# Kernel optimization log

Hardware: AMD Instinct MI355X
Metric: run time of the kernel (lower is better)

The kernel has to match this reference:

```python
import jax, jax.numpy as jnp
import numpy as np

ALPHA = 0.99
EPS = 1e-12
INIT_HI = -60.0
INIT_LO = -90.0
VAR0 = 40.0 ** 2


def setup_inputs() -> dict:
    key = jax.random.key(0)
    x = jax.random.normal(key, (256, 4000, 64), dtype=jnp.float32)
    return {"x": x}


def reference(x) -> jnp.ndarray:
    B, T, F = x.shape
    step = (INIT_LO - INIT_HI) / (F - 1)
    mu0 = INIT_HI + jnp.arange(F, dtype=x.dtype) * step          # [F]
    mu0 = jnp.broadcast_to(mu0[None, :], (B, F))                  # [B, F]
    var0 = jnp.full((B, F), VAR0, dtype=x.dtype)

    def scan_step(carry, xt):
        mu, var = carry
        mu = ALPHA * mu + (1.0 - ALPHA) * xt
        var = ALPHA * var + (1.0 - ALPHA) * (xt - mu) ** 2        # dynamic_var=True
        out = (xt - mu) / (jnp.sqrt(var) + EPS)
        return (mu, var), out

    xt_seq = jnp.swapaxes(x, 0, 1)                                # [T, B, F]
    _, out_seq = jax.lax.scan(scan_step, (mu0, var0), xt_seq)
    return jnp.swapaxes(out_seq, 0, 1)                            # [B, T, F]
```

## Files before the change

kernel.cpp:

```cpp
#include <hip/hip_runtime.h>
#include <math.h>

#define ALPHA   0.99f
#define ONE_M   0.01f
#define T_LEN   4000
#define F_DIM   64
#define TT      160
#define NTILE   25
#define LTC     5
#define NC      32
#define NPC     5
#define NTHREADS 512
#define ROWF    68
#define SLABF   (20 * ROWF)

typedef float f32x4 __attribute__((ext_vector_type(4)));

#define LGKM_BAR()                                                    \
  do { asm volatile("s_waitcnt lgkmcnt(0)" ::: "memory");             \
       __builtin_amdgcn_sched_barrier(0);                             \
       __builtin_amdgcn_s_barrier();                                  \
       __builtin_amdgcn_sched_barrier(0); } while (0)

#define WAVE_FENCE()                                                  \
  do { asm volatile("s_waitcnt lgkmcnt(0)" ::: "memory");             \
       __builtin_amdgcn_sched_barrier(0); } while (0)

#define TILE_BODY(VC, VN, kk)                                               \
  {                                                                         \
    const size_t tb = bbase + (size_t)(kk) * TT * F_DIM;                    \
     \
    if ((kk) + 1 < NTILE) {                                                 \
      _Pragma("unroll")                                                     \
      for (int r = 0; r < NPC; ++r)                                         \
        VN[r] = *(const f32x4*)(x + tb + (size_t)TT * F_DIM + woff          \
                                + (size_t)r * 256 + (size_t)lw * 4);        \
    }                                                                       \
         \
    _Pragma("unroll")                                                       \
    for (int r = 0; r < NPC; ++r)                                           \
      *(f32x4*)&slab[(4 * r + cl) * ROWF + g * 4] = VC[r];                  \
    WAVE_FENCE();                \
           \
    {                                                                       \
      f32x4 m = 0.f, sp = 0.f, su = 0.f;                                    \
      _Pragma("unroll")                                                     \
      for (int j = 0; j < LTC; ++j) {                                       \
        f32x4 xi = *(const f32x4*)&slab[(LTC * cl + j) * ROWF + g * 4];     \
        m = ALPHA * m + ONE_M * xi;                                         \
        f32x4 u = xi - m;                                                   \
        sp = ALPHA * sp + ONE_M * (u * u);                                  \
        su = su + u;                                                        \
      }                                                                     \
      *(f32x4*)&s_m [c * F_DIM + g * 4] = m;                                \
      *(f32x4*)&s_sp[c * F_DIM + g * 4] = sp;                               \
      *(f32x4*)&s_su[c * F_DIM + g * 4] = su;                               \
    }                                                                       \
    LGKM_BAR();                            \
       \
    if (tid < F_DIM) {                                                      \
      float mu = cmu, var = cvar;                                           \
      for (int cc = 0; cc < NC; ++cc) {                                     \
        float mm = s_m [cc * F_DIM + tid];                                  \
        float pp = s_sp[cc * F_DIM + tid];                                  \
        float uu = s_su[cc * F_DIM + tid];                                  \
        s_m [cc * F_DIM + tid] = mu;                    \
        s_sp[cc * F_DIM + tid] = var;                                       \
        float mun = AL * mu + mm;                                           \
        var = AL * var + pp + (C2 * uu) * mu + RR * mu * mu;                \
        mu = mun;                                                           \
      }                                                                     \
      cmu = mu; cvar = var;                                                 \
    }                                                                       \
    LGKM_BAR();   \
      \
    {                                                                       \
      f32x4 mu2  = *(const f32x4*)&s_m [c * F_DIM + g * 4];                 \
      f32x4 var2 = *(const f32x4*)&s_sp[c * F_DIM + g * 4];                 \
      _Pragma("unroll")                                                     \
      for (int j = 0; j < LTC; ++j) {                                       \
        float* rowp = &slab[(LTC * cl + j) * ROWF + g * 4];                 \
        f32x4 xi = *(const f32x4*)rowp;                                     \
        mu2 = ALPHA * mu2 + ONE_M * xi;                                     \
        f32x4 d = xi - mu2;                                                 \
        var2 = ALPHA * var2 + ONE_M * (d * d);                              \
        f32x4 o;                                                            \
        o[0] = d[0] * __builtin_amdgcn_rsqf(var2[0]);                       \
        o[1] = d[1] * __builtin_amdgcn_rsqf(var2[1]);                       \
        o[2] = d[2] * __builtin_amdgcn_rsqf(var2[2]);                       \
        o[3] = d[3] * __builtin_amdgcn_rsqf(var2[3]);                       \
        *(f32x4*)rowp = o;                                                  \
      }                                                                     \
    }                                                                       \
    WAVE_FENCE();                \
     \
    _Pragma("unroll")                                                       \
    for (int r = 0; r < NPC; ++r) {                                         \
      f32x4 oc = *(const f32x4*)&slab[(4 * r + cl) * ROWF + g * 4];         \
      *(f32x4*)(out + tb + woff + (size_t)r * 256 + (size_t)lw * 4) = oc;   \
    }                                                                       \
    WAVE_FENCE();       \
  }

__global__ __launch_bounds__(NTHREADS, 4)
void erbnorm_kernel(const float* __restrict__ x, float* __restrict__ out, float aL) {
    const int b   = blockIdx.x;
    const int tid = threadIdx.x;
    const int w   = tid >> 6;
    const int lw  = tid & 63;
    const int c   = tid >> 4;
    const int cl  = (tid >> 4) & 3;
    const int g   = tid & 15;
    const size_t woff = (size_t)w * 1280;

    const float AL = aL;
    const float C2 = -2.f * ONE_M * aL;
    const float RR = ALPHA * aL * (1.f - aL);

    __shared__ __align__(16) float lds_img[8 * SLABF];
    __shared__ float s_m [NC * F_DIM];
    __shared__ float s_sp[NC * F_DIM];
    __shared__ float s_su[NC * F_DIM];
    float* slab = &lds_img[w * SLABF];

    const size_t bbase = (size_t)b * T_LEN * F_DIM;

    float cmu  = -60.f + (float)tid * (-30.f / 63.f);
    float cvar = 1600.f;

    f32x4 vA[NPC], vB[NPC];
#pragma unroll
    for (int r = 0; r < NPC; ++r)
        vA[r] = *(const f32x4*)(x + bbase + woff + (size_t)r * 256 + (size_t)lw * 4);

    for (int k2 = 0; k2 < NTILE - 1; k2 += 2) {
        TILE_BODY(vA, vB, k2);
        TILE_BODY(vB, vA, k2 + 1);
    }
    TILE_BODY(vA, vB, NTILE - 1);
}

extern "C" void kernel_launch(void* const* d_in, const int* in_sizes, int n_in,
                              void* d_out, int out_size, void* d_ws, size_t ws_size,
                              hipStream_t stream) {
    const float* x = (const float*)d_in[0];
    float* out = (float*)d_out;
    const float aL = (float)pow(0.99, (double)LTC);
    hipLaunchKernelGGL(erbnorm_kernel, dim3(256), dim3(NTHREADS), 0, stream,
                       x, out, aL);
}
```

Before: 114.8 us.

## Add dedicated scan wave and software-pipeline chunk scan across tiles

```diff
diff --git a/kernel.cpp b/kernel.cpp
--- a/kernel.cpp
+++ b/kernel.cpp
@@ -10,7 +10,8 @@
 #define LTC     5
 #define NC      32
 #define NPC     5
-#define NTHREADS 512
+#define NWT     512
+#define NTHREADS 576
 #define ROWF    68
 #define SLABF   (20 * ROWF)
 
@@ -26,83 +27,89 @@
   do { asm volatile("s_waitcnt lgkmcnt(0)" ::: "memory");             \
        __builtin_amdgcn_sched_barrier(0); } while (0)
 
-#define TILE_BODY(VC, VN, kk)                                               \
+#define BODY(VX, SMC, SPC, SUC, SMP, SPP, SUP, ii)                          \
   {                                                                         \
-    const size_t tb = bbase + (size_t)(kk) * TT * F_DIM;                    \
-     \
-    if ((kk) + 1 < NTILE) {                                                 \
-      _Pragma("unroll")                                                     \
-      for (int r = 0; r < NPC; ++r)                                         \
-        VN[r] = *(const f32x4*)(x + tb + (size_t)TT * F_DIM + woff          \
-                                + (size_t)r * 256 + (size_t)lw * 4);        \
-    }                                                                       \
-         \
-    _Pragma("unroll")                                                       \
-    for (int r = 0; r < NPC; ++r)                                           \
-      *(f32x4*)&slab[(4 * r + cl) * ROWF + g * 4] = VC[r];                  \
-    WAVE_FENCE();                \
-           \
-    {                                                                       \
-      f32x4 m = 0.f, sp = 0.f, su = 0.f;                                    \
-      _Pragma("unroll")                                                     \
-      for (int j = 0; j < LTC; ++j) {                                       \
-        f32x4 xi = *(const f32x4*)&slab[(LTC * cl + j) * ROWF + g * 4];     \
-        m = ALPHA * m + ONE_M * xi;                                         \
-        f32x4 u = xi - m;                                                   \
-        sp = ALPHA * sp + ONE_M * (u * u);                                  \
-        su = su + u;                                                        \
+    LGKM_BAR();                                                             \
+    if (tid >= NWT) {                                                       \
+        \
+      if ((ii) < NTILE) {                                                   \
+        float mu = cmu, var = cvar;                                         \
+        for (int cc = 0; cc < NC; ++cc) {                                   \
+          float mm = SMC[cc * F_DIM + f8];                                  \
+          float pp = SPC[cc * F_DIM + f8];                                  \
+          float uu = SUC[cc * F_DIM + f8];                                  \
+          SMC[cc * F_DIM + f8] = mu;                    \
+          SPC[cc * F_DIM + f8] = var;                                       \
+          float mun = AL * mu + mm;                                         \
+          var = AL * var + pp + (C2 * uu) * mu + RR * mu * mu;              \
+          mu = mun;                                                         \
+        }                                                                   \
+        cmu = mu; cvar = var;                                               \
       }                                                                     \
-      *(f32x4*)&s_m [c * F_DIM + g * 4] = m;                                \
-      *(f32x4*)&s_sp[c * F_DIM + g * 4] = sp;                               \
-      *(f32x4*)&s_su[c * F_DIM + g * 4] = su;                               \
-    }                                                                       \
-    LGKM_BAR();                            \
-       \
-    if (tid < F_DIM) {                                                      \
-      float mu = cmu, var = cvar;                                           \
-      for (int cc = 0; cc < NC; ++cc) {                                     \
-        float mm = s_m [cc * F_DIM + tid];                                  \
-        float pp = s_sp[cc * F_DIM + tid];                                  \
-        float uu = s_su[cc * F_DIM + tid];                                  \
-        s_m [cc * F_DIM + tid] = mu;                    \
-        s_sp[cc * F_DIM + tid] = var;                                       \
-        float mun = AL * mu + mm;                                           \
-        var = AL * var + pp + (C2 * uu) * mu + RR * mu * mu;                \
-        mu = mun;                                                           \
+    } else {                                                                \
+      if ((ii) > 0) {                                                       \
+                    \
+        f32x4 mu2  = *(const f32x4*)&SMP[c * F_DIM + g * 4];                \
+        f32x4 var2 = *(const f32x4*)&SPP[c * F_DIM + g * 4];                \
+        _Pragma("unroll")                                                   \
+        for (int j = 0; j < LTC; ++j) {                                     \
+          f32x4 xi = VX[j];                                                 \
+          mu2 = ALPHA * mu2 + ONE_M * xi;                                   \
+          f32x4 d = xi - mu2;                                               \
+          var2 = ALPHA * var2 + ONE_M * (d * d);                            \
+          f32x4 o;                                                          \
+          o[0] = d[0] * __builtin_amdgcn_rsqf(var2[0]);                     \
+          o[1] = d[1] * __builtin_amdgcn_rsqf(var2[1]);                     \
+          o[2] = d[2] * __builtin_amdgcn_rsqf(var2[2]);                     \
+          o[3] = d[3] * __builtin_amdgcn_rsqf(var2[3]);                     \
+          *(f32x4*)&slab[(LTC * cl + j) * ROWF + g * 4] = o;                \
+        }                                                                   \
+        WAVE_FENCE();                \
+                \
+        _Pragma("unroll")                                                   \
+        for (int r = 0; r < NPC; ++r) {                                     \
+          f32x4 oc = *(const f32x4*)&slab[(4 * r + cl) * ROWF + g * 4];     \
+          __builtin_nontemporal_store(oc,                                   \
+              (f32x4*)(out + bbase + (size_t)((ii) - 1) * TT * F_DIM        \
+                       + woff + (size_t)r * 256 + (size_t)lw * 4));         \
+        }                                                                   \
+        WAVE_FENCE();               \
       }                                                                     \
-      cmu = mu; cvar = var;                                                 \
-    }                                                                       \
-    LGKM_BAR();   \
-      \
-    {                                                                       \
-      f32x4 mu2  = *(const f32x4*)&s_m [c * F_DIM + g * 4];                 \
-      f32x4 var2 = *(const f32x4*)&s_sp[c * F_DIM + g * 4];                 \
-      _Pragma("unroll")                                                     \
-      for (int j = 0; j < LTC; ++j) {                                       \
-        float* rowp = &slab[(LTC * cl + j) * ROWF + g * 4];                 \
-        f32x4 xi = *(const f32x4*)rowp;                                     \
-        mu2 = ALPHA * mu2 + ONE_M * xi;                                     \
-        f32x4 d = xi - mu2;                                                 \
-        var2 = ALPHA * var2 + ONE_M * (d * d);                              \
-        f32x4 o;                                                            \
-        o[0] = d[0] * __builtin_amdgcn_rsqf(var2[0]);                       \
-        o[1] = d[1] * __builtin_amdgcn_rsqf(var2[1]);                       \
-        o[2] = d[2] * __builtin_amdgcn_rsqf(var2[2]);                       \
-        o[3] = d[3] * __builtin_amdgcn_rsqf(var2[3]);                       \
-        *(f32x4*)rowp = o;                                                  \
+      if ((ii) + 1 < NTILE) {                                               \
+                       \
+        _Pragma("unroll")                                                   \
+        for (int r = 0; r < NPC; ++r)                                       \
+          *(f32x4*)&slab[(4 * r + cl) * ROWF + g * 4] = vN[r];              \
+        WAVE_FENCE();                \
+                                         \
+        if ((ii) + 2 < NTILE) {                                             \
+          _Pragma("unroll")                                                 \
+          for (int r = 0; r < NPC; ++r)                                     \
+            vN[r] = __builtin_nontemporal_load(                             \
+                (const f32x4*)(x + bbase + (size_t)((ii) + 2) * TT * F_DIM  \
+                               + woff + (size_t)r * 256 + (size_t)lw * 4)); \
+        }                                                                   \
+                  \
+        {                                                                   \
+          f32x4 m = 0.f, sp = 0.f, su = 0.f;                                \
+          _Pragma("unroll")                                                 \
+          for (int j = 0; j < LTC; ++j) {                                   \
+            VX[j] = *(const f32x4*)&slab[(LTC * cl + j) * ROWF + g * 4];    \
+            f32x4 xi = VX[j];                                               \
+            m = ALPHA * m + ONE_M * xi;                                     \
+            f32x4 u = xi - m;                                               \
+            sp = ALPHA * sp + ONE_M * (u * u);                              \
+            su = su + u;                                                    \
+          }                                                                 \
+          *(f32x4*)&SMP[c * F_DIM + g * 4] = m;                             \
+          *(f32x4*)&SPP[c * F_DIM + g * 4] = sp;                            \
+          *(f32x4*)&SUP[c * F_DIM + g * 4] = su;                            \
+        }                                                                   \
       }                                                                     \
     }                                                                       \
-    WAVE_FENCE();                \
-     \
-    _Pragma("unroll")                                                       \
-    for (int r = 0; r < NPC; ++r) {                                         \
-      f32x4 oc = *(const f32x4*)&slab[(4 * r + cl) * ROWF + g * 4];         \
-      *(f32x4*)(out + tb + woff + (size_t)r * 256 + (size_t)lw * 4) = oc;   \
-    }                                                                       \
-    WAVE_FENCE();       \
   }
 
-__global__ __launch_bounds__(NTHREADS, 4)
+__global__ __launch_bounds__(NTHREADS, 3)
 void erbnorm_kernel(const float* __restrict__ x, float* __restrict__ out, float aL) {
     const int b   = blockIdx.x;
     const int tid = threadIdx.x;
@@ -111,6 +118,7 @@
     const int c   = tid >> 4;
     const int cl  = (tid >> 4) & 3;
     const int g   = tid & 15;
+    const int f8  = tid & 63;
     const size_t woff = (size_t)w * 1280;
 
     const float AL = aL;
@@ -118,26 +126,53 @@
     const float RR = ALPHA * aL * (1.f - aL);
 
     __shared__ __align__(16) float lds_img[8 * SLABF];
-    __shared__ float s_m [NC * F_DIM];
-    __shared__ float s_sp[NC * F_DIM];
-    __shared__ float s_su[NC * F_DIM];
-    float* slab = &lds_img[w * SLABF];
+    __shared__ float s_m0[NC * F_DIM], s_sp0[NC * F_DIM], s_su0[NC * F_DIM];
+    __shared__ float s_m1[NC * F_DIM], s_sp1[NC * F_DIM], s_su1[NC * F_DIM];
+    float* slab = &lds_img[(w < 8 ? w : 0) * SLABF];
 
     const size_t bbase = (size_t)b * T_LEN * F_DIM;
 
-    float cmu  = -60.f + (float)tid * (-30.f / 63.f);
+    float cmu  = -60.f + (float)f8 * (-30.f / 63.f);
     float cvar = 1600.f;
 
-    f32x4 vA[NPC], vB[NPC];
+    f32x4 vN[NPC];
+    f32x4 vxE[LTC], vxO[LTC];
+
+    if (tid < NWT) {
 #pragma unroll
-    for (int r = 0; r < NPC; ++r)
-        vA[r] = *(const f32x4*)(x + bbase + woff + (size_t)r * 256 + (size_t)lw * 4);
+        for (int r = 0; r < NPC; ++r)
+            vN[r] = __builtin_nontemporal_load(
+                (const f32x4*)(x + bbase + woff + (size_t)r * 256 + (size_t)lw * 4));
+#pragma unroll
+        for (int r = 0; r < NPC; ++r)
+            *(f32x4*)&slab[(4 * r + cl) * ROWF + g * 4] = vN[r];
+        WAVE_FENCE();
+        {
+            f32x4 m = 0.f, sp = 0.f, su = 0.f;
+#pragma unroll
+            for (int j = 0; j < LTC; ++j) {
+                vxE[j] = *(const f32x4*)&slab[(LTC * cl + j) * ROWF + g * 4];
+                f32x4 xi = vxE[j];
+                m = ALPHA * m + ONE_M * xi;
+                f32x4 u = xi - m;
+                sp = ALPHA * sp + ONE_M * (u * u);
+                su = su + u;
+            }
+            *(f32x4*)&s_m0 [c * F_DIM + g * 4] = m;
+            *(f32x4*)&s_sp0[c * F_DIM + g * 4] = sp;
+            *(f32x4*)&s_su0[c * F_DIM + g * 4] = su;
+        }
+#pragma unroll
+        for (int r = 0; r < NPC; ++r)
+            vN[r] = __builtin_nontemporal_load(
+                (const f32x4*)(x + bbase + (size_t)TT * F_DIM
+                               + woff + (size_t)r * 256 + (size_t)lw * 4));
+    }
 
-    for (int k2 = 0; k2 < NTILE - 1; k2 += 2) {
-        TILE_BODY(vA, vB, k2);
-        TILE_BODY(vB, vA, k2 + 1);
+    for (int i2 = 0; i2 <= NTILE; i2 += 2) {
+        BODY(vxO, s_m0, s_sp0, s_su0, s_m1, s_sp1, s_su1, i2);
+        BODY(vxE, s_m1, s_sp1, s_su1, s_m0, s_sp0, s_su0, i2 + 1);
     }
-    TILE_BODY(vA, vB, NTILE - 1);
 }
 
 extern "C" void kernel_launch(void* const* d_in, const int* in_sizes, int n_in,
```

New measurement: 272.3 us. 2.37x slower.
